# Kernel optimization log

Measured on AMD Instinct MI355X. Metric: run time of the kernel, lower is better.

The kernel has to match this reference:

```python
import jax, jax.numpy as jnp
import numpy as np

NUM_HEADS = 8
NUM_GROUPS = 8
EPS = 1e-5


def group_norm(x, gamma, beta):
    # x: [B, C, H, W]; normalize over (C//G, H, W) per group
    B, C, H, W = x.shape
    xg = x.reshape(B, NUM_GROUPS, C // NUM_GROUPS, H, W)
    mean = jnp.mean(xg, axis=(2, 3, 4), keepdims=True)
    var = jnp.var(xg, axis=(2, 3, 4), keepdims=True)
    xg = (xg - mean) * jax.lax.rsqrt(var + EPS)
    x = xg.reshape(B, C, H, W)
    return x * gamma[None, :, None, None] + beta[None, :, None, None]


def setup_inputs() -> dict:
    key = jax.random.key(0)
    ks = jax.random.split(key, 10)
    B, C, H, W = 16, 512, 32, 32
    s = 0.02
    return {
        "x": jax.random.normal(ks[0], (B, C, H, W), jnp.float32),
        "wq": jax.random.normal(ks[1], (C, C), jnp.float32) * s,
        "bq": jnp.zeros((C,), jnp.float32),
        "wk": jax.random.normal(ks[2], (C, C), jnp.float32) * s,
        "bk": jnp.zeros((C,), jnp.float32),
        "wv": jax.random.normal(ks[3], (C, C), jnp.float32) * s,
        "bv": jnp.zeros((C,), jnp.float32),
        "wo": jax.random.normal(ks[4], (C, C), jnp.float32) * s,
        "bo": jnp.zeros((C,), jnp.float32),
        "gamma": jnp.ones((C,), jnp.float32),
        "beta": jnp.zeros((C,), jnp.float32),
    }


def reference(x, wq, bq, wk, bk, wv, bv, wo, bo, gamma, beta):
    B, C, H, W = x.shape
    Hh = NUM_HEADS
    Dh = C // Hh
    N = H * W
    scale = Dh ** (-0.5)

    residual = x
    xn = group_norm(x, gamma, beta).reshape(B, C, N)  # [B, C, N]

    # Conv1d kernel-size-1 == channel matmul: out[b,o,n] = sum_i w[o,i] x[b,i,n] + b[o]
    q = jnp.einsum('oi,bin->bon', wq, xn) + bq[None, :, None]
    k = jnp.einsum('oi,bin->bon', wk, xn) + bk[None, :, None]
    v = jnp.einsum('oi,bin->bon', wv, xn) + bv[None, :, None]

    q = q.reshape(B, Hh, Dh, N)
    k = k.reshape(B, Hh, Dh, N)
    v = v.reshape(B, Hh, Dh, N)

    attn = jnp.einsum('bhdn,bhdm->bhnm', q, k) * scale  # [B, H, N, N]
    attn = jax.nn.softmax(attn, axis=-1)
    out = jnp.einsum('bhnm,bhdm->bhdn', attn, v)  # [B, H, Dh, N]

    out = out.reshape(B, C, N)
    out = jnp.einsum('oi,bin->bon', wo, out) + bo[None, :, None]
    return out.reshape(B, C, H, W) + residual
```

## Files before the change

### kernel.cpp

```cpp
#include <hip/hip_runtime.h>
#include <hip/hip_bf16.h>

#define BB 16
#define CC 512
#define NN 1024
#define GG 8
#define HHH 8
#define DH 64

typedef __bf16 bf16x8 __attribute__((ext_vector_type(8)));
typedef float f32x4 __attribute__((ext_vector_type(4)));
typedef float f32x16 __attribute__((ext_vector_type(16)));
typedef unsigned int u32x4 __attribute__((ext_vector_type(4)));

#define QSCALE 0.18033688011116027f

__device__ __forceinline__ unsigned short bfb(float f) {
    __hip_bfloat16 h = __float2bfloat16(f);
    return __builtin_bit_cast(unsigned short, h);
}

__device__ __forceinline__ bf16x8 ldb8(const void* p) {
    return *reinterpret_cast<const bf16x8*>(p);
}

__device__ __forceinline__ unsigned int cvtpk(float lo, float hi) {
    unsigned int r;
    asm("v_cvt_pk_bf16_f32 %0, %1, %2" : "=v"(r) : "v"(lo), "v"(hi));
    return r;
}

typedef const __attribute__((address_space(1))) unsigned int* gas_ptr;
typedef __attribute__((address_space(3))) unsigned int* las_ptr;
__device__ __forceinline__ void gload_lds16(const void* g, void* l) {
    __builtin_amdgcn_global_load_lds((gas_ptr)g, (las_ptr)l, 16, 0, 0);
}

__global__ __launch_bounds__(256) void wconv_kernel(
    const float4* __restrict__ wq, const float4* __restrict__ wk,
    const float4* __restrict__ wv, const float4* __restrict__ wo,
    ushort4* __restrict__ oq, ushort4* __restrict__ ok2,
    ushort4* __restrict__ ov, ushort4* __restrict__ oo) {
    int i = blockIdx.x * 256 + threadIdx.x;
    float4 a;
    ushort4 r;
    a = wq[i]; r.x = bfb(a.x); r.y = bfb(a.y); r.z = bfb(a.z); r.w = bfb(a.w); oq[i] = r;
    a = wk[i]; r.x = bfb(a.x); r.y = bfb(a.y); r.z = bfb(a.z); r.w = bfb(a.w); ok2[i] = r;
    a = wv[i]; r.x = bfb(a.x); r.y = bfb(a.y); r.z = bfb(a.z); r.w = bfb(a.w); ov[i] = r;
    a = wo[i]; r.x = bfb(a.x); r.y = bfb(a.y); r.z = bfb(a.z); r.w = bfb(a.w); oo[i] = r;
}

__global__ __launch_bounds__(256) void gn_kernel(
    const float* __restrict__ x, const float* __restrict__ gamma,
    const float* __restrict__ beta, unsigned short* __restrict__ xnT) {
    int b = blockIdx.x >> 3, g = blockIdx.x & 7;
    const float* xg = x + ((size_t)b * CC + g * 64) * NN;
    int t = threadIdx.x;

    float s = 0.f, s2 = 0.f;
    for (int i = 0; i < 64; ++i) {
        float4 v = reinterpret_cast<const float4*>(xg)[t + i * 256];
        s += v.x + v.y + v.z + v.w;
        s2 += v.x * v.x + v.y * v.y + v.z * v.z + v.w * v.w;
    }
    #pragma unroll
    for (int m = 1; m < 64; m <<= 1) {
        s += __shfl_xor(s, m);
        s2 += __shfl_xor(s2, m);
    }
    __shared__ float red[2][4];
    int wid = t >> 6;
    if ((t & 63) == 0) { red[0][wid] = s; red[1][wid] = s2; }
    __syncthreads();
    s = red[0][0] + red[0][1] + red[0][2] + red[0][3];
    s2 = red[1][0] + red[1][1] + red[1][2] + red[1][3];
    float mean = s * (1.f / 65536.f);
    float var = s2 * (1.f / 65536.f) - mean * mean;
    float rstd = rsqrtf(var + 1e-5f);

    __shared__ unsigned short tile[64][68];
    for (int nt = 0; nt < 16; ++nt) {
        __syncthreads();
        #pragma unroll
        for (int p = 0; p < 4; ++p) {
            int cc = p * 16 + (t >> 4);
            int nn = (t & 15) * 4;
            float4 v = *reinterpret_cast<const float4*>(&xg[(size_t)cc * NN + nt * 64 + nn]);
            float ga = gamma[g * 64 + cc], be = beta[g * 64 + cc];
            float aa = rstd * ga;
            float c0 = be - mean * aa;
            ushort4 pk;
            pk.x = bfb(v.x * aa + c0);
            pk.y = bfb(v.y * aa + c0);
            pk.z = bfb(v.z * aa + c0);
            pk.w = bfb(v.w * aa + c0);
            *reinterpret_cast<ushort4*>(&tile[cc][nn]) = pk;
        }
        __syncthreads();
        #pragma unroll
        for (int p = 0; p < 16; ++p) {
            int nn = p * 4 + (t >> 6);
            int cc = t & 63;
            xnT[((size_t)b * NN + nt * 64 + nn) * CC + g * 64 + cc] = tile[cc][nn];
        }
    }
}

__global__ __launch_bounds__(256, 2) void qkv2_kernel(
    const unsigned short* __restrict__ wqb, const unsigned short* __restrict__ wkb,
    const unsigned short* __restrict__ wvb,
    const float* __restrict__ bq, const float* __restrict__ bk, const float* __restrict__ bv,
    const unsigned short* __restrict__ xnT,
    unsigned short* __restrict__ qt, unsigned short* __restrict__ kt,
    unsigned short* __restrict__ vv) {
    int wg = blockIdx.x;
    int xcd = wg & 7, local = wg >> 3;
    int mloc = local / 12;
    int rem = local - mloc * 12;
    int n_tile = rem / 3;
    int p = rem - n_tile * 3;
    int m_tile = xcd * 16 + mloc;

    const unsigned short* w = (p == 0) ? wqb : (p == 1) ? wkb : wvb;
    const float* bias = (p == 0) ? bq : (p == 1) ? bk : bv;
    int row0 = m_tile * 128;
    int o0t = n_tile * 128;

    __shared__ __align__(16) char As[2][16384];
    __shared__ __align__(16) char Bs[2][16384];

    int t = threadIdx.x;
    int lane = t & 63, wid = t >> 6;
    int Rl = lane >> 3;
    int csw = ((lane & 7) ^ Rl) << 4;

    const char* Ag = (const char*)xnT + (size_t)row0 * 1024;
    const char* Bg = (const char*)w + (size_t)o0t * 1024;

    #pragma unroll
    for (int j = 0; j < 4; ++j) {
        int ii = wid * 4 + j;
        size_t ro = (size_t)(ii * 8 + Rl) * 1024 + csw;
        gload_lds16(Ag + ro, &As[0][ii * 1024]);
        gload_lds16(Bg + ro, &Bs[0][ii * 1024]);
    }
    __syncthreads();

    int wr = wid & 1, wc = wid >> 1;
    int lr = lane & 15, lg = lane >> 4;
    f32x4 acc[4][4] = {};

    for (int ks = 0; ks < 8; ++ks) {
        int cb_ = ks & 1;
        if (ks < 7) {
            int k0 = (ks + 1) * 64;
            #pragma unroll
            for (int j = 0; j < 4; ++j) {
                int ii = wid * 4 + j;
                size_t ro = (size_t)(ii * 8 + Rl) * 1024 + k0 * 2 + csw;
                gload_lds16(Ag + ro, &As[cb_ ^ 1][ii * 1024]);
                gload_lds16(Bg + ro, &Bs[cb_ ^ 1][ii * 1024]);
            }
        }
        const char* al = As[cb_];
        const char* bl = Bs[cb_];
        #pragma unroll
        for (int kk = 0; kk < 2; ++kk) {
            bf16x8 wf[4], xf[4];
            #pragma unroll
            for (int r = 0; r < 4; ++r) {
                int row = wc * 64 + r * 16 + lr;
                wf[r] = ldb8(bl + row * 128 + (((kk * 4 + lg) ^ (row & 7)) << 4));
            }
            #pragma unroll
            for (int c = 0; c < 4; ++c) {
                int row = wr * 64 + c * 16 + lr;
                xf[c] = ldb8(al + row * 128 + (((kk * 4 + lg) ^ (row & 7)) << 4));
            }
            __builtin_amdgcn_s_setprio(1);
            #pragma unroll
            for (int r = 0; r < 4; ++r)
                #pragma unroll
                for (int c = 0; c < 4; ++c)
                    acc[r][c] = __builtin_amdgcn_mfma_f32_16x16x32_bf16(wf[r], xf[c], acc[r][c], 0, 0, 0);
            __builtin_amdgcn_s_setprio(0);
        }
        __syncthreads();
    }

    #pragma unroll
    for (int r = 0; r < 4; ++r) {
        int o0 = o0t + wc * 64 + r * 16 + lg * 4;
        #pragma unroll
        for (int c = 0; c < 4; ++c) {
            int grow = row0 + wr * 64 + c * 16 + lr;
            int b = grow >> 10, n = grow & 1023;
            float v0 = acc[r][c][0] + bias[o0 + 0];
            float v1 = acc[r][c][1] + bias[o0 + 1];
            float v2 = acc[r][c][2] + bias[o0 + 2];
            float v3 = acc[r][c][3] + bias[o0 + 3];
            if (p < 2) {
                if (p == 0) { v0 *= QSCALE; v1 *= QSCALE; v2 *= QSCALE; v3 *= QSCALE; }
                unsigned short* outp = (p == 0) ? qt : kt;
                int h = o0 >> 6, d = o0 & 63;
                ushort4 pk;
                pk.x = bfb(v0); pk.y = bfb(v1); pk.z = bfb(v2); pk.w = bfb(v3);
                *reinterpret_cast<ushort4*>(outp + ((size_t)(b * HHH + h) * NN + n) * DH + d) = pk;
            } else {
                vv[((size_t)b * CC + o0 + 0) * NN + n] = bfb(v0);
                vv[((size_t)b * CC + o0 + 1) * NN + n] = bfb(v1);
                vv[((size_t)b * CC + o0 + 2) * NN + n] = bfb(v2);
                vv[((size_t)b * CC + o0 + 3) * NN + n] = bfb(v3);
            }
        }
    }
}

__global__ __launch_bounds__(256, 2) void attn4_kernel(
    const unsigned short* __restrict__ qt, const unsigned short* __restrict__ kt,
    const unsigned short* __restrict__ vv, unsigned short* __restrict__ aoT) {
    int wg = blockIdx.x;
    int bh = ((wg >> 6) << 3) + (wg & 7);
    int qt8 = (wg >> 3) & 7;
    int b = bh >> 3, h = bh & 7;
    int lane = threadIdx.x & 63, wid = threadIdx.x >> 6;
    int nl = lane & 31, hi = lane >> 5;
    int n = qt8 * 128 + wid * 32 + nl;

    const unsigned short* Qb = qt + (size_t)bh * NN * DH;
    const unsigned short* Kb = kt + (size_t)bh * NN * DH;
    const unsigned short* Vb = vv + ((size_t)b * CC + h * DH) * NN;

    __shared__ __align__(16) char smem[2][16384];

    const unsigned short* Qp = Qb + (size_t)n * DH + hi * 8;
    bf16x8 qf[4];
    qf[0] = ldb8(Qp);
    qf[1] = ldb8(Qp + 16);
    qf[2] = ldb8(Qp + 32);
    qf[3] = ldb8(Qp + 48);

    int Rl = lane >> 3;
    int cs16 = 16 * ((lane & 7) ^ Rl);
    const char* Kc = (const char*)Kb;
    const char* Vc = (const char*)Vb;

    #pragma unroll
    for (int j = 0; j < 2; ++j) {
        int ii = 2 * wid + j;
        int R = ii * 8 + Rl;
        gload_lds16(Kc + (size_t)R * 128 + cs16, &smem[0][ii * 1024]);
        gload_lds16(Vc + (size_t)R * 2048 + cs16, &smem[0][8192 + ii * 1024]);
    }
    __syncthreads();

    f32x16 o0 = {}, o1 = {};
    float l_i = 0.f;
    int cur = 0;

    for (int mt = 0; mt < 16; ++mt) {
        if (mt < 15) {
            int m0n = (mt + 1) * 64;
            #pragma unroll
            for (int j = 0; j < 2; ++j) {
                int ii = 2 * wid + j;
                int R = ii * 8 + Rl;
                gload_lds16(Kc + (size_t)(m0n + R) * 128 + cs16, &smem[cur ^ 1][ii * 1024]);
                gload_lds16(Vc + (size_t)R * 2048 + (size_t)m0n * 2 + cs16,
                            &smem[cur ^ 1][8192 + ii * 1024]);
            }
        }

        const char* kl = &smem[cur][0];
        const char* vl = &smem[cur][8192];
        int swz = (nl & 7) << 4;
        int rowA = nl * 128, rowB = (nl + 32) * 128;

        bf16x8 ka[4], kbf[4];
        #pragma unroll
        for (int ks = 0; ks < 4; ++ks) {
            int cb = (hi * 16 + ks * 32) ^ swz;
            ka[ks]  = ldb8(kl + rowA + cb);
            kbf[ks] = ldb8(kl + rowB + cb);
        }

        f32x16 s0 = {}, s1 = {};
        __builtin_amdgcn_s_setprio(1);
        #pragma unroll
        for (int ks = 0; ks < 4; ++ks) {
            s0 = __builtin_amdgcn_mfma_f32_32x32x16_bf16(ka[ks], qf[ks], s0, 0, 0, 0);
            s1 = __builtin_amdgcn_mfma_f32_32x32x16_bf16(kbf[ks], qf[ks], s1, 0, 0, 0);
        }
        __builtin_amdgcn_s_setprio(0);

        bf16x8 va[4], vbf[4];
        #pragma unroll
        for (int ks = 0; ks < 4; ++ks) {
            int cb = (hi * 16 + ks * 32) ^ swz;
            va[ks]  = ldb8(vl + rowA + cb);
            vbf[ks] = ldb8(vl + rowB + cb);
        }

        #pragma unroll
        for (int e = 0; e < 16; ++e) s0[e] = __builtin_amdgcn_exp2f(s0[e]);
        #pragma unroll
        for (int e = 0; e < 16; ++e) s1[e] = __builtin_amdgcn_exp2f(s1[e]);
        float ts[16];
        #pragma unroll
        for (int e = 0; e < 16; ++e) ts[e] = s0[e] + s1[e];
        #pragma unroll
        for (int st = 8; st; st >>= 1)
            #pragma unroll
            for (int e = 0; e < st; ++e) ts[e] += ts[e + st];
        l_i += ts[0];

        unsigned pA = cvtpk(s0[0], s0[1]), pB = cvtpk(s0[4], s0[5]);
        asm("v_permlane32_swap_b32 %0, %1" : "+v"(pA), "+v"(pB));
        unsigned pC = cvtpk(s0[2], s0[3]), pD = cvtpk(s0[6], s0[7]);
        asm("v_permlane32_swap_b32 %0, %1" : "+v"(pC), "+v"(pD));
        unsigned pE = cvtpk(s0[8], s0[9]), pF = cvtpk(s0[12], s0[13]);
        asm("v_permlane32_swap_b32 %0, %1" : "+v"(pE), "+v"(pF));
        unsigned pG = cvtpk(s0[10], s0[11]), pH = cvtpk(s0[14], s0[15]);
        asm("v_permlane32_swap_b32 %0, %1" : "+v"(pG), "+v"(pH));
        u32x4 w00 = {pA, pC, pB, pD};
        u32x4 w01 = {pE, pG, pF, pH};
        unsigned qA = cvtpk(s1[0], s1[1]), qB = cvtpk(s1[4], s1[5]);
        asm("v_permlane32_swap_b32 %0, %1" : "+v"(qA), "+v"(qB));
        unsigned qC = cvtpk(s1[2], s1[3]), qD = cvtpk(s1[6], s1[7]);
        asm("v_permlane32_swap_b32 %0, %1" : "+v"(qC), "+v"(qD));
        unsigned qE = cvtpk(s1[8], s1[9]), qF = cvtpk(s1[12], s1[13]);
        asm("v_permlane32_swap_b32 %0, %1" : "+v"(qE), "+v"(qF));
        unsigned qG = cvtpk(s1[10], s1[11]), qH = cvtpk(s1[14], s1[15]);
        asm("v_permlane32_swap_b32 %0, %1" : "+v"(qG), "+v"(qH));
        u32x4 w10 = {qA, qC, qB, qD};
        u32x4 w11 = {qE, qG, qF, qH};

        bf16x8 pa00 = __builtin_bit_cast(bf16x8, w00);
        bf16x8 pa01 = __builtin_bit_cast(bf16x8, w01);
        bf16x8 pa10 = __builtin_bit_cast(bf16x8, w10);
        bf16x8 pa11 = __builtin_bit_cast(bf16x8, w11);

        __builtin_amdgcn_s_setprio(1);
        o0 = __builtin_amdgcn_mfma_f32_32x32x16_bf16(va[0], pa00, o0, 0, 0, 0);
        o0 = __builtin_amdgcn_mfma_f32_32x32x16_bf16(va[1], pa01, o0, 0, 0, 0);
        o0 = __builtin_amdgcn_mfma_f32_32x32x16_bf16(va[2], pa10, o0, 0, 0, 0);
        o0 = __builtin_amdgcn_mfma_f32_32x32x16_bf16(va[3], pa11, o0, 0, 0, 0);
        o1 = __builtin_amdgcn_mfma_f32_32x32x16_bf16(vbf[0], pa00, o1, 0, 0, 0);
        o1 = __builtin_amdgcn_mfma_f32_32x32x16_bf16(vbf[1], pa01, o1, 0, 0, 0);
        o1 = __builtin_amdgcn_mfma_f32_32x32x16_bf16(vbf[2], pa10, o1, 0, 0, 0);
        o1 = __builtin_amdgcn_mfma_f32_32x32x16_bf16(vbf[3], pa11, o1, 0, 0, 0);
        __builtin_amdgcn_s_setprio(0);

        __syncthreads();
        cur ^= 1;
    }

    float l = l_i + __shfl_xor(l_i, 32);
    float inv = 1.f / l;
    unsigned short* op = aoT + ((size_t)b * NN + n) * CC + h * DH;
    #pragma unroll
    for (int q = 0; q < 4; ++q) {
        ushort4 pk;
        pk.x = bfb(o0[4 * q + 0] * inv);
        pk.y = bfb(o0[4 * q + 1] * inv);
        pk.z = bfb(o0[4 * q + 2] * inv);
        pk.w = bfb(o0[4 * q + 3] * inv);
        *reinterpret_cast<ushort4*>(op + q * 8 + hi * 4) = pk;
        ushort4 pk2;
        pk2.x = bfb(o1[4 * q + 0] * inv);
        pk2.y = bfb(o1[4 * q + 1] * inv);
        pk2.z = bfb(o1[4 * q + 2] * inv);
        pk2.w = bfb(o1[4 * q + 3] * inv);
        *reinterpret_cast<ushort4*>(op + 32 + q * 8 + hi * 4) = pk2;
    }
}

__global__ __launch_bounds__(256, 2) void oproj2_kernel(
    const unsigned short* __restrict__ wob, const float* __restrict__ bo,
    const unsigned short* __restrict__ aoT, const float* __restrict__ x,
    float* __restrict__ out) {
    int wg = blockIdx.x;
    int xcd = wg & 7, local = wg >> 3;
    int mloc = local >> 2;
    int n_tile = local & 3;
    int m_tile = xcd * 16 + mloc;
    int row0 = m_tile * 128;
    int o0t = n_tile * 128;

    __shared__ __align__(16) char As[2][16384];
    __shared__ __align__(16) char Bs[2][16384];

    int t = threadIdx.x;
    int lane = t & 63, wid = t >> 6;
    int Rl = lane >> 3;
    int csw = ((lane & 7) ^ Rl) << 4;

    const char* Ag = (const char*)aoT + (size_t)row0 * 1024;
    const char* Bg = (const char*)wob + (size_t)o0t * 1024;

    #pragma unroll
    for (int j = 0; j < 4; ++j) {
        int ii = wid * 4 + j;
        size_t ro = (size_t)(ii * 8 + Rl) * 1024 + csw;
        gload_lds16(Ag + ro, &As[0][ii * 1024]);
        gload_lds16(Bg + ro, &Bs[0][ii * 1024]);
    }
    __syncthreads();

    int wr = wid & 1, wc = wid >> 1;
    int lr = lane & 15, lg = lane >> 4;
    f32x4 acc[4][4] = {};

    for (int ks = 0; ks < 8; ++ks) {
        int cb_ = ks & 1;
        if (ks < 7) {
            int k0 = (ks + 1) * 64;
            #pragma unroll
            for (int j = 0; j < 4; ++j) {
                int ii = wid * 4 + j;
                size_t ro = (size_t)(ii * 8 + Rl) * 1024 + k0 * 2 + csw;
                gload_lds16(Ag + ro, &As[cb_ ^ 1][ii * 1024]);
                gload_lds16(Bg + ro, &Bs[cb_ ^ 1][ii * 1024]);
            }
        }
        const char* al = As[cb_];
        const char* bl = Bs[cb_];
        #pragma unroll
        for (int kk = 0; kk < 2; ++kk) {
            bf16x8 wf[4], xf[4];
            #pragma unroll
            for (int r = 0; r < 4; ++r) {
                int row = wc * 64 + r * 16 + lr;
                wf[r] = ldb8(bl + row * 128 + (((kk * 4 + lg) ^ (row & 7)) << 4));
            }
            #pragma unroll
            for (int c = 0; c < 4; ++c) {
                int row = wr * 64 + c * 16 + lr;
                xf[c] = ldb8(al + row * 128 + (((kk * 4 + lg) ^ (row & 7)) << 4));
            }
            __builtin_amdgcn_s_setprio(1);
            #pragma unroll
            for (int r = 0; r < 4; ++r)
                #pragma unroll
                for (int c = 0; c < 4; ++c)
                    acc[r][c] = __builtin_amdgcn_mfma_f32_16x16x32_bf16(wf[r], xf[c], acc[r][c], 0, 0, 0);
            __builtin_amdgcn_s_setprio(0);
        }
        __syncthreads();
    }

    #pragma unroll
    for (int r = 0; r < 4; ++r) {
        int o0 = o0t + wc * 64 + r * 16 + lg * 4;
        #pragma unroll
        for (int c = 0; c < 4; ++c) {
            int grow = row0 + wr * 64 + c * 16 + lr;
            int b = grow >> 10, n = grow & 1023;
            #pragma unroll
            for (int j = 0; j < 4; ++j) {
                size_t idx = ((size_t)b * CC + o0 + j) * NN + n;
                out[idx] = acc[r][c][j] + bo[o0 + j] + x[idx];
            }
        }
    }
}

extern "C" void kernel_launch(void* const* d_in, const int* in_sizes, int n_in,
                              void* d_out, int out_size, void* d_ws, size_t ws_size,
                              hipStream_t stream) {
    const float* x     = (const float*)d_in[0];
    const float* wq    = (const float*)d_in[1];
    const float* bq    = (const float*)d_in[2];
    const float* wk    = (const float*)d_in[3];
    const float* bk    = (const float*)d_in[4];
    const float* wv    = (const float*)d_in[5];
    const float* bv    = (const float*)d_in[6];
    const float* wo    = (const float*)d_in[7];
    const float* bo    = (const float*)d_in[8];
    const float* gamma = (const float*)d_in[9];
    const float* beta  = (const float*)d_in[10];

    char* ws = (char*)d_ws;
    const size_t WSZ = (size_t)CC * CC * 2;
    const size_t TEN = (size_t)BB * NN * CC * 2;
    unsigned short* wqb = (unsigned short*)(ws);
    unsigned short* wkb = (unsigned short*)(ws + WSZ);
    unsigned short* wvb = (unsigned short*)(ws + 2 * WSZ);
    unsigned short* wob = (unsigned short*)(ws + 3 * WSZ);
    unsigned short* xnT = (unsigned short*)(ws + 4 * WSZ);
    unsigned short* qt  = (unsigned short*)(ws + 4 * WSZ + TEN);
    unsigned short* kt  = (unsigned short*)(ws + 4 * WSZ + 2 * TEN);
    unsigned short* vv  = (unsigned short*)(ws + 4 * WSZ + 3 * TEN);
    unsigned short* aoT = (unsigned short*)(ws + 4 * WSZ + 4 * TEN);

    wconv_kernel<<<dim3(256), dim3(256), 0, stream>>>(
        (const float4*)wq, (const float4*)wk, (const float4*)wv, (const float4*)wo,
        (ushort4*)wqb, (ushort4*)wkb, (ushort4*)wvb, (ushort4*)wob);
    gn_kernel<<<dim3(128), dim3(256), 0, stream>>>(x, gamma, beta, xnT);
    qkv2_kernel<<<dim3(1536), dim3(256), 0, stream>>>(
        wqb, wkb, wvb, bq, bk, bv, xnT, qt, kt, vv);
    attn4_kernel<<<dim3(1024), dim3(256), 0, stream>>>(qt, kt, vv, aoT);
    oproj2_kernel<<<dim3(512), dim3(256), 0, stream>>>(wob, bo, aoT, x, (float*)d_out);
}
```

Baseline: 128.9 us.

## Process two query tiles per wave and triple-buffer K/V staging in attention

Each attention workgroup now handles 256 queries (two 32-row query blocks per wave) instead of 128, so every K/V tile loaded into LDS is reused twice and the grid halves to 512 blocks. The K/V prefetch moves from double to triple buffering, using explicit vmcnt waits and a single barrier per iteration. This cuts global K/V traffic and barrier count per unit of work, at the cost of more accumulator registers (four output tiles), more LDS, and fewer blocks for occupancy and load balance.

After: 127.2 us. No clear change (-1.3%).

```diff
diff --git a/kernel.cpp b/kernel.cpp
--- a/kernel.cpp
+++ b/kernel.cpp
@@ -216,63 +216,67 @@
     }
 }
 
-__global__ __launch_bounds__(256, 2) void attn4_kernel(
+__global__ __launch_bounds__(256, 2) void attn5_kernel(
     const unsigned short* __restrict__ qt, const unsigned short* __restrict__ kt,
     const unsigned short* __restrict__ vv, unsigned short* __restrict__ aoT) {
     int wg = blockIdx.x;
-    int bh = ((wg >> 6) << 3) + (wg & 7);
-    int qt8 = (wg >> 3) & 7;
+    int xcd = wg & 7;
+    int qp = (wg >> 3) & 3;
+    int bh = ((wg >> 5) << 3) | xcd;
     int b = bh >> 3, h = bh & 7;
     int lane = threadIdx.x & 63, wid = threadIdx.x >> 6;
     int nl = lane & 31, hi = lane >> 5;
-    int n = qt8 * 128 + wid * 32 + nl;
+    int nA = qp * 256 + wid * 32 + nl;
+    int nB = nA + 128;
 
     const unsigned short* Qb = qt + (size_t)bh * NN * DH;
     const unsigned short* Kb = kt + (size_t)bh * NN * DH;
     const unsigned short* Vb = vv + ((size_t)b * CC + h * DH) * NN;
 
-    __shared__ __align__(16) char smem[2][16384];
-
-    const unsigned short* Qp = Qb + (size_t)n * DH + hi * 8;
-    bf16x8 qf[4];
-    qf[0] = ldb8(Qp);
-    qf[1] = ldb8(Qp + 16);
-    qf[2] = ldb8(Qp + 32);
-    qf[3] = ldb8(Qp + 48);
+    __shared__ __align__(16) char smem[3][16384];
+
+    const unsigned short* QpA = Qb + (size_t)nA * DH + hi * 8;
+    const unsigned short* QpB = Qb + (size_t)nB * DH + hi * 8;
+    bf16x8 qfA[4], qfB[4];
+    #pragma unroll
+    for (int ks = 0; ks < 4; ++ks) {
+        qfA[ks] = ldb8(QpA + ks * 16);
+        qfB[ks] = ldb8(QpB + ks * 16);
+    }
 
     int Rl = lane >> 3;
     int cs16 = 16 * ((lane & 7) ^ Rl);
     const char* Kc = (const char*)Kb;
     const char* Vc = (const char*)Vb;
 
-    #pragma unroll
-    for (int j = 0; j < 2; ++j) {
-        int ii = 2 * wid + j;
-        int R = ii * 8 + Rl;
-        gload_lds16(Kc + (size_t)R * 128 + cs16, &smem[0][ii * 1024]);
-        gload_lds16(Vc + (size_t)R * 2048 + cs16, &smem[0][8192 + ii * 1024]);
-    }
-    __syncthreads();
-
-    f32x16 o0 = {}, o1 = {};
-    float l_i = 0.f;
-    int cur = 0;
+    #define STAGE(tt, buf)                                                        \
+        {                                                                         \
+            int m0_ = (tt) * 64;                                                  \
+            _Pragma("unroll")                                                     \
+            for (int j = 0; j < 2; ++j) {                                         \
+                int ii = 2 * wid + j;                                             \
+                int R = ii * 8 + Rl;                                              \
+                gload_lds16(Kc + (size_t)(m0_ + R) * 128 + cs16,                  \
+                            &smem[buf][ii * 1024]);                               \
+                gload_lds16(Vc + (size_t)R * 2048 + (size_t)m0_ * 2 + cs16,       \
+                            &smem[buf][8192 + ii * 1024]);                        \
+            }                                                                     \
+        }
+
+    STAGE(0, 0);
+    STAGE(1, 1);
+
+    f32x16 oA0 = {}, oA1 = {}, oB0 = {}, oB1 = {};
+    float lA = 0.f, lB = 0.f;
 
     for (int mt = 0; mt < 16; ++mt) {
-        if (mt < 15) {
-            int m0n = (mt + 1) * 64;
-            #pragma unroll
-            for (int j = 0; j < 2; ++j) {
-                int ii = 2 * wid + j;
-                int R = ii * 8 + Rl;
-                gload_lds16(Kc + (size_t)(m0n + R) * 128 + cs16, &smem[cur ^ 1][ii * 1024]);
-                gload_lds16(Vc + (size_t)R * 2048 + (size_t)m0n * 2 + cs16,
-                            &smem[cur ^ 1][8192 + ii * 1024]);
-            }
-        }
-
-        const char* kl = &smem[cur][0];
-        const char* vl = &smem[cur][8192];
+        if (mt < 15) asm volatile("s_waitcnt vmcnt(4)" ::: "memory");
+        else         asm volatile("s_waitcnt vmcnt(0)" ::: "memory");
+        __builtin_amdgcn_s_barrier();
+        if (mt < 14) STAGE(mt + 2, (mt + 2) % 3);
+
+        const char* kl = &smem[mt % 3][0];
+        const char* vl = &smem[mt % 3][8192];
         int swz = (nl & 7) << 4;
         int rowA = nl * 128, rowB = (nl + 32) * 128;
 
@@ -284,12 +288,14 @@
             kbf[ks] = ldb8(kl + rowB + cb);
         }
 
-        f32x16 s0 = {}, s1 = {};
+        f32x16 sA0 = {}, sA1 = {}, sB0 = {}, sB1 = {};
         __builtin_amdgcn_s_setprio(1);
         #pragma unroll
         for (int ks = 0; ks < 4; ++ks) {
-            s0 = __builtin_amdgcn_mfma_f32_32x32x16_bf16(ka[ks], qf[ks], s0, 0, 0, 0);
-            s1 = __builtin_amdgcn_mfma_f32_32x32x16_bf16(kbf[ks], qf[ks], s1, 0, 0, 0);
+            sA0 = __builtin_amdgcn_mfma_f32_32x32x16_bf16(ka[ks],  qfA[ks], sA0, 0, 0, 0);
+            sA1 = __builtin_amdgcn_mfma_f32_32x32x16_bf16(kbf[ks], qfA[ks], sA1, 0, 0, 0);
+            sB0 = __builtin_amdgcn_mfma_f32_32x32x16_bf16(ka[ks],  qfB[ks], sB0, 0, 0, 0);
+            sB1 = __builtin_amdgcn_mfma_f32_32x32x16_bf16(kbf[ks], qfB[ks], sB1, 0, 0, 0);
         }
         __builtin_amdgcn_s_setprio(0);
 
@@ -302,76 +308,137 @@
         }
 
         #pragma unroll
-        for (int e = 0; e < 16; ++e) s0[e] = __builtin_amdgcn_exp2f(s0[e]);
-        #pragma unroll
-        for (int e = 0; e < 16; ++e) s1[e] = __builtin_amdgcn_exp2f(s1[e]);
-        float ts[16];
-        #pragma unroll
-        for (int e = 0; e < 16; ++e) ts[e] = s0[e] + s1[e];
-        #pragma unroll
-        for (int st = 8; st; st >>= 1)
-            #pragma unroll
-            for (int e = 0; e < st; ++e) ts[e] += ts[e + st];
-        l_i += ts[0];
-
-        unsigned pA = cvtpk(s0[0], s0[1]), pB = cvtpk(s0[4], s0[5]);
-        asm("v_permlane32_swap_b32 %0, %1" : "+v"(pA), "+v"(pB));
-        unsigned pC = cvtpk(s0[2], s0[3]), pD = cvtpk(s0[6], s0[7]);
-        asm("v_permlane32_swap_b32 %0, %1" : "+v"(pC), "+v"(pD));
-        unsigned pE = cvtpk(s0[8], s0[9]), pF = cvtpk(s0[12], s0[13]);
-        asm("v_permlane32_swap_b32 %0, %1" : "+v"(pE), "+v"(pF));
-        unsigned pG = cvtpk(s0[10], s0[11]), pH = cvtpk(s0[14], s0[15]);
-        asm("v_permlane32_swap_b32 %0, %1" : "+v"(pG), "+v"(pH));
-        u32x4 w00 = {pA, pC, pB, pD};
-        u32x4 w01 = {pE, pG, pF, pH};
-        unsigned qA = cvtpk(s1[0], s1[1]), qB = cvtpk(s1[4], s1[5]);
-        asm("v_permlane32_swap_b32 %0, %1" : "+v"(qA), "+v"(qB));
-        unsigned qC = cvtpk(s1[2], s1[3]), qD = cvtpk(s1[6], s1[7]);
-        asm("v_permlane32_swap_b32 %0, %1" : "+v"(qC), "+v"(qD));
-        unsigned qE = cvtpk(s1[8], s1[9]), qF = cvtpk(s1[12], s1[13]);
-        asm("v_permlane32_swap_b32 %0, %1" : "+v"(qE), "+v"(qF));
-        unsigned qG = cvtpk(s1[10], s1[11]), qH = cvtpk(s1[14], s1[15]);
-        asm("v_permlane32_swap_b32 %0, %1" : "+v"(qG), "+v"(qH));
-        u32x4 w10 = {qA, qC, qB, qD};
-        u32x4 w11 = {qE, qG, qF, qH};
-
-        bf16x8 pa00 = __builtin_bit_cast(bf16x8, w00);
-        bf16x8 pa01 = __builtin_bit_cast(bf16x8, w01);
-        bf16x8 pa10 = __builtin_bit_cast(bf16x8, w10);
-        bf16x8 pa11 = __builtin_bit_cast(bf16x8, w11);
-
-        __builtin_amdgcn_s_setprio(1);
-        o0 = __builtin_amdgcn_mfma_f32_32x32x16_bf16(va[0], pa00, o0, 0, 0, 0);
-        o0 = __builtin_amdgcn_mfma_f32_32x32x16_bf16(va[1], pa01, o0, 0, 0, 0);
-        o0 = __builtin_amdgcn_mfma_f32_32x32x16_bf16(va[2], pa10, o0, 0, 0, 0);
-        o0 = __builtin_amdgcn_mfma_f32_32x32x16_bf16(va[3], pa11, o0, 0, 0, 0);
-        o1 = __builtin_amdgcn_mfma_f32_32x32x16_bf16(vbf[0], pa00, o1, 0, 0, 0);
-        o1 = __builtin_amdgcn_mfma_f32_32x32x16_bf16(vbf[1], pa01, o1, 0, 0, 0);
-        o1 = __builtin_amdgcn_mfma_f32_32x32x16_bf16(vbf[2], pa10, o1, 0, 0, 0);
-        o1 = __builtin_amdgcn_mfma_f32_32x32x16_bf16(vbf[3], pa11, o1, 0, 0, 0);
-        __builtin_amdgcn_s_setprio(0);
-
-        __syncthreads();
-        cur ^= 1;
-    }
-
-    float l = l_i + __shfl_xor(l_i, 32);
-    float inv = 1.f / l;
-    unsigned short* op = aoT + ((size_t)b * NN + n) * CC + h * DH;
+        for (int e = 0; e < 16; ++e) sA0[e] = __builtin_amdgcn_exp2f(sA0[e]);
+        #pragma unroll
+        for (int e = 0; e < 16; ++e) sA1[e] = __builtin_amdgcn_exp2f(sA1[e]);
+        {
+            float ts[16];
+            #pragma unroll
+            for (int e = 0; e < 16; ++e) ts[e] = sA0[e] + sA1[e];
+            #pragma unroll
+            for (int st = 8; st; st >>= 1)
+                #pragma unroll
+                for (int e = 0; e < st; ++e) ts[e] += ts[e + st];
+            lA += ts[0];
+        }
+        {
+            unsigned pA = cvtpk(sA0[0], sA0[1]), pB = cvtpk(sA0[4], sA0[5]);
+            asm("v_permlane32_swap_b32 %0, %1" : "+v"(pA), "+v"(pB));
+            unsigned pC = cvtpk(sA0[2], sA0[3]), pD = cvtpk(sA0[6], sA0[7]);
+            asm("v_permlane32_swap_b32 %0, %1" : "+v"(pC), "+v"(pD));
+            unsigned pE = cvtpk(sA0[8], sA0[9]), pF = cvtpk(sA0[12], sA0[13]);
+            asm("v_permlane32_swap_b32 %0, %1" : "+v"(pE), "+v"(pF));
+            unsigned pG = cvtpk(sA0[10], sA0[11]), pH = cvtpk(sA0[14], sA0[15]);
+            asm("v_permlane32_swap_b32 %0, %1" : "+v"(pG), "+v"(pH));
+            u32x4 w00 = {pA, pC, pB, pD};
+            u32x4 w01 = {pE, pG, pF, pH};
+            unsigned qA = cvtpk(sA1[0], sA1[1]), qB = cvtpk(sA1[4], sA1[5]);
+            asm("v_permlane32_swap_b32 %0, %1" : "+v"(qA), "+v"(qB));
+            unsigned qC = cvtpk(sA1[2], sA1[3]), qD = cvtpk(sA1[6], sA1[7]);
+            asm("v_permlane32_swap_b32 %0, %1" : "+v"(qC), "+v"(qD));
+            unsigned qE = cvtpk(sA1[8], sA1[9]), qF = cvtpk(sA1[12], sA1[13]);
+            asm("v_permlane32_swap_b32 %0, %1" : "+v"(qE), "+v"(qF));
+            unsigned qG = cvtpk(sA1[10], sA1[11]), qH = cvtpk(sA1[14], sA1[15]);
+            asm("v_permlane32_swap_b32 %0, %1" : "+v"(qG), "+v"(qH));
+            u32x4 w10 = {qA, qC, qB, qD};
+            u32x4 w11 = {qE, qG, qF, qH};
+            bf16x8 pa00 = __builtin_bit_cast(bf16x8, w00);
+            bf16x8 pa01 = __builtin_bit_cast(bf16x8, w01);
+            bf16x8 pa10 = __builtin_bit_cast(bf16x8, w10);
+            bf16x8 pa11 = __builtin_bit_cast(bf16x8, w11);
+            __builtin_amdgcn_s_setprio(1);
+            oA0 = __builtin_amdgcn_mfma_f32_32x32x16_bf16(va[0],  pa00, oA0, 0, 0, 0);
+            oA0 = __builtin_amdgcn_mfma_f32_32x32x16_bf16(va[1],  pa01, oA0, 0, 0, 0);
+            oA0 = __builtin_amdgcn_mfma_f32_32x32x16_bf16(va[2],  pa10, oA0, 0, 0, 0);
+            oA0 = __builtin_amdgcn_mfma_f32_32x32x16_bf16(va[3],  pa11, oA0, 0, 0, 0);
+            oA1 = __builtin_amdgcn_mfma_f32_32x32x16_bf16(vbf[0], pa00, oA1, 0, 0, 0);
+            oA1 = __builtin_amdgcn_mfma_f32_32x32x16_bf16(vbf[1], pa01, oA1, 0, 0, 0);
+            oA1 = __builtin_amdgcn_mfma_f32_32x32x16_bf16(vbf[2], pa10, oA1, 0, 0, 0);
+            oA1 = __builtin_amdgcn_mfma_f32_32x32x16_bf16(vbf[3], pa11, oA1, 0, 0, 0);
+            __builtin_amdgcn_s_setprio(0);
+        }
+
+        #pragma unroll
+        for (int e = 0; e < 16; ++e) sB0[e] = __builtin_amdgcn_exp2f(sB0[e]);
+        #pragma unroll
+        for (int e = 0; e < 16; ++e) sB1[e] = __builtin_amdgcn_exp2f(sB1[e]);
+        {
+            float ts[16];
+            #pragma unroll
+            for (int e = 0; e < 16; ++e) ts[e] = sB0[e] + sB1[e];
+            #pragma unroll
+            for (int st = 8; st; st >>= 1)
+                #pragma unroll
+                for (int e = 0; e < st; ++e) ts[e] += ts[e + st];
+            lB += ts[0];
+        }
+        {
+            unsigned pA = cvtpk(sB0[0], sB0[1]), pB = cvtpk(sB0[4], sB0[5]);
+            asm("v_permlane32_swap_b32 %0, %1" : "+v"(pA), "+v"(pB));
+            unsigned pC = cvtpk(sB0[2], sB0[3]), pD = cvtpk(sB0[6], sB0[7]);
+            asm("v_permlane32_swap_b32 %0, %1" : "+v"(pC), "+v"(pD));
+            unsigned pE = cvtpk(sB0[8], sB0[9]), pF = cvtpk(sB0[12], sB0[13]);
+            asm("v_permlane32_swap_b32 %0, %1" : "+v"(pE), "+v"(pF));
+            unsigned pG = cvtpk(sB0[10], sB0[11]), pH = cvtpk(sB0[14], sB0[15]);
+            asm("v_permlane32_swap_b32 %0, %1" : "+v"(pG), "+v"(pH));
+            u32x4 w00 = {pA, pC, pB, pD};
+            u32x4 w01 = {pE, pG, pF, pH};
+            unsigned qA = cvtpk(sB1[0], sB1[1]), qB = cvtpk(sB1[4], sB1[5]);
+            asm("v_permlane32_swap_b32 %0, %1" : "+v"(qA), "+v"(qB));
+            unsigned qC = cvtpk(sB1[2], sB1[3]), qD = cvtpk(sB1[6], sB1[7]);
+            asm("v_permlane32_swap_b32 %0, %1" : "+v"(qC), "+v"(qD));
+            unsigned qE = cvtpk(sB1[8], sB1[9]), qF = cvtpk(sB1[12], sB1[13]);
+            asm("v_permlane32_swap_b32 %0, %1" : "+v"(qE), "+v"(qF));
+            unsigned qG = cvtpk(sB1[10], sB1[11]), qH = cvtpk(sB1[14], sB1[15]);
+            asm("v_permlane32_swap_b32 %0, %1" : "+v"(qG), "+v"(qH));
+            u32x4 w10 = {qA, qC, qB, qD};
+            u32x4 w11 = {qE, qG, qF, qH};
+            bf16x8 pb00 = __builtin_bit_cast(bf16x8, w00);
+            bf16x8 pb01 = __builtin_bit_cast(bf16x8, w01);
+            bf16x8 pb10 = __builtin_bit_cast(bf16x8, w10);
+            bf16x8 pb11 = __builtin_bit_cast(bf16x8, w11);
+            __builtin_amdgcn_s_setprio(1);
+            oB0 = __builtin_amdgcn_mfma_f32_32x32x16_bf16(va[0],  pb00, oB0, 0, 0, 0);
+            oB0 = __builtin_amdgcn_mfma_f32_32x32x16_bf16(va[1],  pb01, oB0, 0, 0, 0);
+            oB0 = __builtin_amdgcn_mfma_f32_32x32x16_bf16(va[2],  pb10, oB0, 0, 0, 0);
+            oB0 = __builtin_amdgcn_mfma_f32_32x32x16_bf16(va[3],  pb11, oB0, 0, 0, 0);
+            oB1 = __builtin_amdgcn_mfma_f32_32x32x16_bf16(vbf[0], pb00, oB1, 0, 0, 0);
+            oB1 = __builtin_amdgcn_mfma_f32_32x32x16_bf16(vbf[1], pb01, oB1, 0, 0, 0);
+            oB1 = __builtin_amdgcn_mfma_f32_32x32x16_bf16(vbf[2], pb10, oB1, 0, 0, 0);
+            oB1 = __builtin_amdgcn_mfma_f32_32x32x16_bf16(vbf[3], pb11, oB1, 0, 0, 0);
+            __builtin_amdgcn_s_setprio(0);
+        }
+    }
+    #undef STAGE
+
+    float lAm = lA + __shfl_xor(lA, 32);
+    float lBm = lB + __shfl_xor(lB, 32);
+    float invA = 1.f / lAm, invB = 1.f / lBm;
+    unsigned short* opA = aoT + ((size_t)b * NN + nA) * CC + h * DH;
+    unsigned short* opB = aoT + ((size_t)b * NN + nB) * CC + h * DH;
     #pragma unroll
     for (int q = 0; q < 4; ++q) {
         ushort4 pk;
-        pk.x = bfb(o0[4 * q + 0] * inv);
-        pk.y = bfb(o0[4 * q + 1] * inv);
-        pk.z = bfb(o0[4 * q + 2] * inv);
-        pk.w = bfb(o0[4 * q + 3] * inv);
-        *reinterpret_cast<ushort4*>(op + q * 8 + hi * 4) = pk;
-        ushort4 pk2;
-        pk2.x = bfb(o1[4 * q + 0] * inv);
-        pk2.y = bfb(o1[4 * q + 1] * inv);
-        pk2.z = bfb(o1[4 * q + 2] * inv);
-        pk2.w = bfb(o1[4 * q + 3] * inv);
-        *reinterpret_cast<ushort4*>(op + 32 + q * 8 + hi * 4) = pk2;
+        pk.x = bfb(oA0[4 * q + 0] * invA);
+        pk.y = bfb(oA0[4 * q + 1] * invA);
+        pk.z = bfb(oA0[4 * q + 2] * invA);
+        pk.w = bfb(oA0[4 * q + 3] * invA);
+        *reinterpret_cast<ushort4*>(opA + q * 8 + hi * 4) = pk;
+        pk.x = bfb(oA1[4 * q + 0] * invA);
+        pk.y = bfb(oA1[4 * q + 1] * invA);
+        pk.z = bfb(oA1[4 * q + 2] * invA);
+        pk.w = bfb(oA1[4 * q + 3] * invA);
+        *reinterpret_cast<ushort4*>(opA + 32 + q * 8 + hi * 4) = pk;
+        pk.x = bfb(oB0[4 * q + 0] * invB);
+        pk.y = bfb(oB0[4 * q + 1] * invB);
+        pk.z = bfb(oB0[4 * q + 2] * invB);
+        pk.w = bfb(oB0[4 * q + 3] * invB);
+        *reinterpret_cast<ushort4*>(opB + q * 8 + hi * 4) = pk;
+        pk.x = bfb(oB1[4 * q + 0] * invB);
+        pk.y = bfb(oB1[4 * q + 1] * invB);
+        pk.z = bfb(oB1[4 * q + 2] * invB);
+        pk.w = bfb(oB1[4 * q + 3] * invB);
+        *reinterpret_cast<ushort4*>(opB + 32 + q * 8 + hi * 4) = pk;
     }
 }
 
@@ -499,6 +566,6 @@
     gn_kernel<<<dim3(128), dim3(256), 0, stream>>>(x, gamma, beta, xnT);
     qkv2_kernel<<<dim3(1536), dim3(256), 0, stream>>>(
         wqb, wkb, wvb, bq, bk, bv, xnT, qt, kt, vv);
-    attn4_kernel<<<dim3(1024), dim3(256), 0, stream>>>(qt, kt, vv, aoT);
+    attn5_kernel<<<dim3(512), dim3(256), 0, stream>>>(qt, kt, vv, aoT);
     oproj2_kernel<<<dim3(512), dim3(256), 0, stream>>>(wob, bo, aoT, x, (float*)d_out);
 }
```

## Software-pipeline attention with triple-buffered LDS and overlapped QK^T/PV stages

Applied to the files above, without the earlier changes.

Moves the attention kernel from double- to triple-buffered K/V tiles in LDS, prefetching two tiles ahead. The loop is unrolled by two with ping-pong score registers, so the QK^T MFMAs for tile t+1 are issued before the exp/convert/PV work of tile t, overlapping matrix and vector work. It also splits the row-sum into vector partial sums and raises launch bounds to 3 blocks per CU. The costs are more LDS (48KB per block) and more live registers, which could prevent the higher occupancy or cause spills.

Measured after the change: 207.0 us. +60.6%, slower.

```diff
diff --git a/kernel.cpp b/kernel.cpp
--- a/kernel.cpp
+++ b/kernel.cpp
@@ -216,7 +216,7 @@
     }
 }
 
-__global__ __launch_bounds__(256, 2) void attn4_kernel(
+__global__ __launch_bounds__(256, 3) void attn7_kernel(
     const unsigned short* __restrict__ qt, const unsigned short* __restrict__ kt,
     const unsigned short* __restrict__ vv, unsigned short* __restrict__ aoT) {
     int wg = blockIdx.x;
@@ -231,7 +231,7 @@
     const unsigned short* Kb = kt + (size_t)bh * NN * DH;
     const unsigned short* Vb = vv + ((size_t)b * CC + h * DH) * NN;
 
-    __shared__ __align__(16) char smem[2][16384];
+    __shared__ __align__(16) char smem[3][16384];
 
     const unsigned short* Qp = Qb + (size_t)n * DH + hi * 8;
     bf16x8 qf[4];
@@ -245,116 +245,131 @@
     const char* Kc = (const char*)Kb;
     const char* Vc = (const char*)Vb;
 
-    #pragma unroll
-    for (int j = 0; j < 2; ++j) {
-        int ii = 2 * wid + j;
-        int R = ii * 8 + Rl;
-        gload_lds16(Kc + (size_t)R * 128 + cs16, &smem[0][ii * 1024]);
-        gload_lds16(Vc + (size_t)R * 2048 + cs16, &smem[0][8192 + ii * 1024]);
-    }
-    __syncthreads();
+    #define STAGE(tt, buf)                                                        \
+        {                                                                         \
+            int m0_ = (tt) * 64;                                                  \
+            _Pragma("unroll")                                                     \
+            for (int j = 0; j < 2; ++j) {                                         \
+                int ii = 2 * wid + j;                                             \
+                int R = ii * 8 + Rl;                                              \
+                gload_lds16(Kc + (size_t)(m0_ + R) * 128 + cs16,                  \
+                            &smem[buf][ii * 1024]);                               \
+                gload_lds16(Vc + (size_t)R * 2048 + (size_t)m0_ * 2 + cs16,       \
+                            &smem[buf][8192 + ii * 1024]);                        \
+            }                                                                     \
+        }
+
+    int swz = (nl & 7) << 4;
+    int rowA = nl * 128, rowB = (nl + 32) * 128;
+
+    #define QK_READ(SN0, SN1, TT)                                                 \
+        {                                                                         \
+            const char* kl_ = &smem[(TT) % 3][0];                                 \
+            bf16x8 k0_ = ldb8(kl_ + rowA + ((hi * 16 +  0) ^ swz));               \
+            bf16x8 k1_ = ldb8(kl_ + rowA + ((hi * 16 + 32) ^ swz));               \
+            bf16x8 k2_ = ldb8(kl_ + rowA + ((hi * 16 + 64) ^ swz));               \
+            bf16x8 k3_ = ldb8(kl_ + rowA + ((hi * 16 + 96) ^ swz));               \
+            bf16x8 l0_ = ldb8(kl_ + rowB + ((hi * 16 +  0) ^ swz));               \
+            bf16x8 l1_ = ldb8(kl_ + rowB + ((hi * 16 + 32) ^ swz));               \
+            bf16x8 l2_ = ldb8(kl_ + rowB + ((hi * 16 + 64) ^ swz));               \
+            bf16x8 l3_ = ldb8(kl_ + rowB + ((hi * 16 + 96) ^ swz));               \
+            __builtin_amdgcn_s_setprio(1);                                        \
+            SN0 = __builtin_amdgcn_mfma_f32_32x32x16_bf16(k0_, qf[0], SN0, 0, 0, 0); \
+            SN1 = __builtin_amdgcn_mfma_f32_32x32x16_bf16(l0_, qf[0], SN1, 0, 0, 0); \
+            SN0 = __builtin_amdgcn_mfma_f32_32x32x16_bf16(k1_, qf[1], SN0, 0, 0, 0); \
+            SN1 = __builtin_amdgcn_mfma_f32_32x32x16_bf16(l1_, qf[1], SN1, 0, 0, 0); \
+            SN0 = __builtin_amdgcn_mfma_f32_32x32x16_bf16(k2_, qf[2], SN0, 0, 0, 0); \
+            SN1 = __builtin_amdgcn_mfma_f32_32x32x16_bf16(l2_, qf[2], SN1, 0, 0, 0); \
+            SN0 = __builtin_amdgcn_mfma_f32_32x32x16_bf16(k3_, qf[3], SN0, 0, 0, 0); \
+            SN1 = __builtin_amdgcn_mfma_f32_32x32x16_bf16(l3_, qf[3], SN1, 0, 0, 0); \
+            __builtin_amdgcn_s_setprio(0);                                        \
+        }
+
+    #define BODY(SC0, SC1, SN0, SN1, T)                                           \
+    {                                                                             \
+        asm volatile("s_waitcnt lgkmcnt(0)" ::: "memory");                        \
+        asm volatile("s_waitcnt vmcnt(0)" ::: "memory");                          \
+        __builtin_amdgcn_s_barrier();                                             \
+        if ((T) < 14) STAGE((T) + 2, ((T) + 2) % 3);                              \
+        if ((T) < 15) {                                                           \
+            SN0 = (f32x16){};                                                     \
+            SN1 = (f32x16){};                                                     \
+            QK_READ(SN0, SN1, (T) + 1);                                           \
+        }                                                                         \
+        _Pragma("unroll")                                                         \
+        for (int e = 0; e < 16; ++e) SC0[e] = __builtin_amdgcn_exp2f(SC0[e]);     \
+        _Pragma("unroll")                                                         \
+        for (int e = 0; e < 16; ++e) SC1[e] = __builtin_amdgcn_exp2f(SC1[e]);     \
+        _Pragma("unroll")                                                         \
+        for (int e = 0; e < 4; ++e) {                                             \
+            tsa[e] += (SC0[e] + SC0[e + 4]) + (SC0[e + 8] + SC0[e + 12]);         \
+            tsb[e] += (SC1[e] + SC1[e + 4]) + (SC1[e + 8] + SC1[e + 12]);         \
+        }                                                                         \
+        unsigned pA = cvtpk(SC0[0], SC0[1]), pB = cvtpk(SC0[4], SC0[5]);          \
+        asm("v_permlane32_swap_b32 %0, %1" : "+v"(pA), "+v"(pB));                 \
+        unsigned pC = cvtpk(SC0[2], SC0[3]), pD = cvtpk(SC0[6], SC0[7]);          \
+        asm("v_permlane32_swap_b32 %0, %1" : "+v"(pC), "+v"(pD));                 \
+        unsigned pE = cvtpk(SC0[8], SC0[9]), pF = cvtpk(SC0[12], SC0[13]);        \
+        asm("v_permlane32_swap_b32 %0, %1" : "+v"(pE), "+v"(pF));                 \
+        unsigned pG = cvtpk(SC0[10], SC0[11]), pH = cvtpk(SC0[14], SC0[15]);      \
+        asm("v_permlane32_swap_b32 %0, %1" : "+v"(pG), "+v"(pH));                 \
+        u32x4 w00 = {pA, pC, pB, pD};                                             \
+        u32x4 w01 = {pE, pG, pF, pH};                                             \
+        unsigned qA = cvtpk(SC1[0], SC1[1]), qB = cvtpk(SC1[4], SC1[5]);          \
+        asm("v_permlane32_swap_b32 %0, %1" : "+v"(qA), "+v"(qB));                 \
+        unsigned qC = cvtpk(SC1[2], SC1[3]), qD = cvtpk(SC1[6], SC1[7]);          \
+        asm("v_permlane32_swap_b32 %0, %1" : "+v"(qC), "+v"(qD));                 \
+        unsigned qE = cvtpk(SC1[8], SC1[9]), qF = cvtpk(SC1[12], SC1[13]);        \
+        asm("v_permlane32_swap_b32 %0, %1" : "+v"(qE), "+v"(qF));                 \
+        unsigned qG = cvtpk(SC1[10], SC1[11]), qH = cvtpk(SC1[14], SC1[15]);      \
+        asm("v_permlane32_swap_b32 %0, %1" : "+v"(qG), "+v"(qH));                 \
+        u32x4 w10 = {qA, qC, qB, qD};                                             \
+        u32x4 w11 = {qE, qG, qF, qH};                                             \
+        bf16x8 pa00 = __builtin_bit_cast(bf16x8, w00);                            \
+        bf16x8 pa01 = __builtin_bit_cast(bf16x8, w01);                            \
+        bf16x8 pa10 = __builtin_bit_cast(bf16x8, w10);                            \
+        bf16x8 pa11 = __builtin_bit_cast(bf16x8, w11);                            \
+        const char* vl_ = &smem[(T) % 3][8192];                                   \
+        bf16x8 va0 = ldb8(vl_ + rowA + ((hi * 16 +  0) ^ swz));                   \
+        bf16x8 va1 = ldb8(vl_ + rowA + ((hi * 16 + 32) ^ swz));                   \
+        bf16x8 va2 = ldb8(vl_ + rowA + ((hi * 16 + 64) ^ swz));                   \
+        bf16x8 va3 = ldb8(vl_ + rowA + ((hi * 16 + 96) ^ swz));                   \
+        bf16x8 vb0 = ldb8(vl_ + rowB + ((hi * 16 +  0) ^ swz));                   \
+        bf16x8 vb1 = ldb8(vl_ + rowB + ((hi * 16 + 32) ^ swz));                   \
+        bf16x8 vb2 = ldb8(vl_ + rowB + ((hi * 16 + 64) ^ swz));                   \
+        bf16x8 vb3 = ldb8(vl_ + rowB + ((hi * 16 + 96) ^ swz));                   \
+        __builtin_amdgcn_s_setprio(1);                                            \
+        o0 = __builtin_amdgcn_mfma_f32_32x32x16_bf16(va0, pa00, o0, 0, 0, 0);     \
+        o0 = __builtin_amdgcn_mfma_f32_32x32x16_bf16(va1, pa01, o0, 0, 0, 0);     \
+        o0 = __builtin_amdgcn_mfma_f32_32x32x16_bf16(va2, pa10, o0, 0, 0, 0);     \
+        o0 = __builtin_amdgcn_mfma_f32_32x32x16_bf16(va3, pa11, o0, 0, 0, 0);     \
+        o1 = __builtin_amdgcn_mfma_f32_32x32x16_bf16(vb0, pa00, o1, 0, 0, 0);     \
+        o1 = __builtin_amdgcn_mfma_f32_32x32x16_bf16(vb1, pa01, o1, 0, 0, 0);     \
+        o1 = __builtin_amdgcn_mfma_f32_32x32x16_bf16(vb2, pa10, o1, 0, 0, 0);     \
+        o1 = __builtin_amdgcn_mfma_f32_32x32x16_bf16(vb3, pa11, o1, 0, 0, 0);     \
+        __builtin_amdgcn_s_setprio(0);                                            \
+    }
+
+    STAGE(0, 0);
+    STAGE(1, 1);
+    asm volatile("s_waitcnt vmcnt(0)" ::: "memory");
+    __builtin_amdgcn_s_barrier();
 
     f32x16 o0 = {}, o1 = {};
-    float l_i = 0.f;
-    int cur = 0;
-
-    for (int mt = 0; mt < 16; ++mt) {
-        if (mt < 15) {
-            int m0n = (mt + 1) * 64;
-            #pragma unroll
-            for (int j = 0; j < 2; ++j) {
-                int ii = 2 * wid + j;
-                int R = ii * 8 + Rl;
-                gload_lds16(Kc + (size_t)(m0n + R) * 128 + cs16, &smem[cur ^ 1][ii * 1024]);
-                gload_lds16(Vc + (size_t)R * 2048 + (size_t)m0n * 2 + cs16,
-                            &smem[cur ^ 1][8192 + ii * 1024]);
-            }
-        }
-
-        const char* kl = &smem[cur][0];
-        const char* vl = &smem[cur][8192];
-        int swz = (nl & 7) << 4;
-        int rowA = nl * 128, rowB = (nl + 32) * 128;
-
-        bf16x8 ka[4], kbf[4];
-        #pragma unroll
-        for (int ks = 0; ks < 4; ++ks) {
-            int cb = (hi * 16 + ks * 32) ^ swz;
-            ka[ks]  = ldb8(kl + rowA + cb);
-            kbf[ks] = ldb8(kl + rowB + cb);
-        }
-
-        f32x16 s0 = {}, s1 = {};
-        __builtin_amdgcn_s_setprio(1);
-        #pragma unroll
-        for (int ks = 0; ks < 4; ++ks) {
-            s0 = __builtin_amdgcn_mfma_f32_32x32x16_bf16(ka[ks], qf[ks], s0, 0, 0, 0);
-            s1 = __builtin_amdgcn_mfma_f32_32x32x16_bf16(kbf[ks], qf[ks], s1, 0, 0, 0);
-        }
-        __builtin_amdgcn_s_setprio(0);
-
-        bf16x8 va[4], vbf[4];
-        #pragma unroll
-        for (int ks = 0; ks < 4; ++ks) {
-            int cb = (hi * 16 + ks * 32) ^ swz;
-            va[ks]  = ldb8(vl + rowA + cb);
-            vbf[ks] = ldb8(vl + rowB + cb);
-        }
-
-        #pragma unroll
-        for (int e = 0; e < 16; ++e) s0[e] = __builtin_amdgcn_exp2f(s0[e]);
-        #pragma unroll
-        for (int e = 0; e < 16; ++e) s1[e] = __builtin_amdgcn_exp2f(s1[e]);
-        float ts[16];
-        #pragma unroll
-        for (int e = 0; e < 16; ++e) ts[e] = s0[e] + s1[e];
-        #pragma unroll
-        for (int st = 8; st; st >>= 1)
-            #pragma unroll
-            for (int e = 0; e < st; ++e) ts[e] += ts[e + st];
-        l_i += ts[0];
-
-        unsigned pA = cvtpk(s0[0], s0[1]), pB = cvtpk(s0[4], s0[5]);
-        asm("v_permlane32_swap_b32 %0, %1" : "+v"(pA), "+v"(pB));
-        unsigned pC = cvtpk(s0[2], s0[3]), pD = cvtpk(s0[6], s0[7]);
-        asm("v_permlane32_swap_b32 %0, %1" : "+v"(pC), "+v"(pD));
-        unsigned pE = cvtpk(s0[8], s0[9]), pF = cvtpk(s0[12], s0[13]);
-        asm("v_permlane32_swap_b32 %0, %1" : "+v"(pE), "+v"(pF));
-        unsigned pG = cvtpk(s0[10], s0[11]), pH = cvtpk(s0[14], s0[15]);
-        asm("v_permlane32_swap_b32 %0, %1" : "+v"(pG), "+v"(pH));
-        u32x4 w00 = {pA, pC, pB, pD};
-        u32x4 w01 = {pE, pG, pF, pH};
-        unsigned qA = cvtpk(s1[0], s1[1]), qB = cvtpk(s1[4], s1[5]);
-        asm("v_permlane32_swap_b32 %0, %1" : "+v"(qA), "+v"(qB));
-        unsigned qC = cvtpk(s1[2], s1[3]), qD = cvtpk(s1[6], s1[7]);
-        asm("v_permlane32_swap_b32 %0, %1" : "+v"(qC), "+v"(qD));
-        unsigned qE = cvtpk(s1[8], s1[9]), qF = cvtpk(s1[12], s1[13]);
-        asm("v_permlane32_swap_b32 %0, %1" : "+v"(qE), "+v"(qF));
-        unsigned qG = cvtpk(s1[10], s1[11]), qH = cvtpk(s1[14], s1[15]);
-        asm("v_permlane32_swap_b32 %0, %1" : "+v"(qG), "+v"(qH));
-        u32x4 w10 = {qA, qC, qB, qD};
-        u32x4 w11 = {qE, qG, qF, qH};
-
-        bf16x8 pa00 = __builtin_bit_cast(bf16x8, w00);
-        bf16x8 pa01 = __builtin_bit_cast(bf16x8, w01);
-        bf16x8 pa10 = __builtin_bit_cast(bf16x8, w10);
-        bf16x8 pa11 = __builtin_bit_cast(bf16x8, w11);
-
-        __builtin_amdgcn_s_setprio(1);
-        o0 = __builtin_amdgcn_mfma_f32_32x32x16_bf16(va[0], pa00, o0, 0, 0, 0);
-        o0 = __builtin_amdgcn_mfma_f32_32x32x16_bf16(va[1], pa01, o0, 0, 0, 0);
-        o0 = __builtin_amdgcn_mfma_f32_32x32x16_bf16(va[2], pa10, o0, 0, 0, 0);
-        o0 = __builtin_amdgcn_mfma_f32_32x32x16_bf16(va[3], pa11, o0, 0, 0, 0);
-        o1 = __builtin_amdgcn_mfma_f32_32x32x16_bf16(vbf[0], pa00, o1, 0, 0, 0);
-        o1 = __builtin_amdgcn_mfma_f32_32x32x16_bf16(vbf[1], pa01, o1, 0, 0, 0);
-        o1 = __builtin_amdgcn_mfma_f32_32x32x16_bf16(vbf[2], pa10, o1, 0, 0, 0);
-        o1 = __builtin_amdgcn_mfma_f32_32x32x16_bf16(vbf[3], pa11, o1, 0, 0, 0);
-        __builtin_amdgcn_s_setprio(0);
-
-        __syncthreads();
-        cur ^= 1;
-    }
-
+    f32x4 tsa = {}, tsb = {};
+    f32x16 sA0 = {}, sA1 = {}, sB0, sB1;
+    QK_READ(sA0, sA1, 0);
+
+    for (int mt = 0; mt < 16; mt += 2) {
+        BODY(sA0, sA1, sB0, sB1, mt);
+        BODY(sB0, sB1, sA0, sA1, mt + 1);
+    }
+    #undef BODY
+    #undef QK_READ
+    #undef STAGE
+
+    float l_i = (tsa[0] + tsa[1]) + (tsa[2] + tsa[3]) +
+                (tsb[0] + tsb[1]) + (tsb[2] + tsb[3]);
     float l = l_i + __shfl_xor(l_i, 32);
     float inv = 1.f / l;
     unsigned short* op = aoT + ((size_t)b * NN + n) * CC + h * DH;
@@ -499,6 +514,6 @@
     gn_kernel<<<dim3(128), dim3(256), 0, stream>>>(x, gamma, beta, xnT);
     qkv2_kernel<<<dim3(1536), dim3(256), 0, stream>>>(
         wqb, wkb, wvb, bq, bk, bv, xnT, qt, kt, vv);
-    attn4_kernel<<<dim3(1024), dim3(256), 0, stream>>>(qt, kt, vv, aoT);
+    attn7_kernel<<<dim3(1024), dim3(256), 0, stream>>>(qt, kt, vv, aoT);
     oproj2_kernel<<<dim3(512), dim3(256), 0, stream>>>(wob, bo, aoT, x, (float*)d_out);
 }
```
